# Optimization experiments

Measured on AMD Instinct MI355X. Metric: run time of the kernel, lower is better.

## Reference

```python
import jax, jax.numpy as jnp
import numpy as np
import math

N_NODES = 100000
N_EDGES = 1600000
D_FEAT = 32
K = 1        # Bernstein index k
N_ORD = 2    # Bernstein order n
COMB = float(math.comb(N_ORD, K))


def setup_inputs() -> dict:
    key = jax.random.key(0)
    k1, k2, k3 = jax.random.split(key, 3)
    feat = jax.random.normal(k1, (N_NODES, D_FEAT), dtype=jnp.float32)
    edge_src = jax.random.randint(k2, (N_EDGES,), 0, N_NODES)
    edge_dst = jax.random.randint(k3, (N_EDGES,), 0, N_NODES)
    return {"feat": feat, "edge_src": edge_src, "edge_dst": edge_dst}


def reference(feat, edge_src, edge_dst):
    # in-degree of each node (copy_u/sum aggregates over incoming edges)
    deg = jax.ops.segment_sum(jnp.ones((N_EDGES,), feat.dtype), edge_dst,
                              num_segments=N_NODES)
    d_invsqrt = jnp.clip(deg, 1.0, None) ** -0.5  # [N]
    d_invsqrt = d_invsqrt[:, None]                 # [N,1]

    def unn_laplacian(x):
        msg = (x * d_invsqrt)[edge_src]            # [E,D]
        agg = jax.ops.segment_sum(msg, edge_dst, num_segments=N_NODES)
        return x - agg * d_invsqrt

    if K == 0:
        h = feat
        for _ in range(N_ORD):
            h = unn_laplacian(h) / 2
            h = feat - h
    elif K == N_ORD:
        h = feat
        for _ in range(N_ORD):
            h = unn_laplacian(h) / 2
    else:
        temp = feat
        for _ in range(K):
            temp = unn_laplacian(temp) / 2
        h = feat
        for _ in range(N_ORD - K):
            h = unn_laplacian(h) / 2
            h = feat - h
        h = temp * h
    return COMB * h
```

## Files before the change

kernel.cpp:

```cpp
#include <hip/hip_runtime.h>

#define N_NODES 100000
#define N_EDGES 1600000
#define D_FEAT 32

#define BSH 7
#define BMASK 127
#define NB 782
#define CAPB 2432

#define P1_BS 512
#define P1_TILE 4096
#define P1_CAP 16


static __device__ __forceinline__ unsigned pack_bf16(float a, float b) {
    unsigned ua = __float_as_uint(a);
    unsigned ub = __float_as_uint(b);
    ua = (ua + 0x7FFFu + ((ua >> 16) & 1u)) >> 16;
    ub = (ub + 0x7FFFu + ((ub >> 16) & 1u)) >> 16;
    return (ua & 0xFFFFu) | (ub << 16);
}

__global__ void init_kernel(int* __restrict__ cursorA) {
    int b = blockIdx.x * blockDim.x + threadIdx.x;
    if (b < NB) cursorA[b] = b * CAPB;
}

__global__ void __launch_bounds__(P1_BS)
bucket_kernel(const int* __restrict__ edge_src,
              const int* __restrict__ edge_dst,
              int* __restrict__ cursorA,
              int* __restrict__ pairs, int n_edges) {
    __shared__ int s_cnt[NB];
    __shared__ int s_base[NB];
    __shared__ int s_off[NB + 1];
    __shared__ int s_buf[NB * P1_CAP];

    int tile = blockIdx.x * P1_TILE;
    if (tile >= n_edges) return;

    for (int b = threadIdx.x; b < NB; b += P1_BS) s_cnt[b] = 0;
    __syncthreads();

    const int4* src4 = reinterpret_cast<const int4*>(edge_src);
    const int4* dst4 = reinterpret_cast<const int4*>(edge_dst);
    int tileq = blockIdx.x * (P1_TILE / 4);
    #pragma unroll
    for (int j = 0; j < P1_TILE / 4 / P1_BS; ++j) {
        int iq = tileq + j * P1_BS + threadIdx.x;
        if (iq * 4 < n_edges) {
            int4 sv = src4[iq];
            int4 dv = dst4[iq];
            int ss[4] = {sv.x, sv.y, sv.z, sv.w};
            int dd[4] = {dv.x, dv.y, dv.z, dv.w};
            #pragma unroll
            for (int u = 0; u < 4; ++u) {
                int b = dd[u] >> BSH;
                int packed = (ss[u] << BSH) | (dd[u] & BMASK);
                int p = atomicAdd(&s_cnt[b], 1);
                if (p < P1_CAP) {
                    s_buf[b * P1_CAP + p] = packed;
                } else {
                    int gp = atomicAdd(&cursorA[b], 1);
                    pairs[gp] = packed;
                }
            }
        }
    }
    __syncthreads();

    for (int b = threadIdx.x; b < NB; b += P1_BS) {
        int c = min(s_cnt[b], P1_CAP);
        s_base[b] = atomicAdd(&cursorA[b], c);
        s_cnt[b] = c;
    }
    __syncthreads();
    if (threadIdx.x == 0) {
        int acc = 0;
        for (int b = 0; b < NB; ++b) { s_off[b] = acc; acc += s_cnt[b]; }
        s_off[NB] = acc;
    }
    __syncthreads();

    int total = s_off[NB];
    for (int t = threadIdx.x; t < total; t += P1_BS) {
        int lo = 0, hi = NB;
        while (hi - lo > 1) {
            int mid = (lo + hi) >> 1;
            if (t >= s_off[mid]) lo = mid; else hi = mid;
        }
        int idx = t - s_off[lo];
        pairs[s_base[lo] + idx] = s_buf[lo * P1_CAP + idx];
    }
}

__global__ void __launch_bounds__(256)
sort_kernel(const int* __restrict__ pairs,
            const int* __restrict__ cursorA,
            const float* __restrict__ feat,
            int* __restrict__ ssrc,
            int2* __restrict__ srange,
            float* __restrict__ dinv,
            unsigned* __restrict__ sfeat) {
    __shared__ int buf[CAPB];
    __shared__ int outb[CAPB];
    __shared__ int h[128];
    __shared__ int sc[128];
    __shared__ int cur[128];
    __shared__ float dv_s[128];

    int b = blockIdx.x;
    int t = threadIdx.x;
    int base = b * CAPB;
    int cnt = min(cursorA[b] - base, CAPB);

    if (t < 128) h[t] = 0;
    __syncthreads();
    for (int i = t; i < cnt; i += 256) {
        int p = pairs[base + i];
        buf[i] = p;
        atomicAdd(&h[p & BMASK], 1);
    }
    __syncthreads();

    int v = 0;
    if (t < 128) { v = h[t]; sc[t] = v; }
    __syncthreads();
    for (int off = 1; off < 128; off <<= 1) {
        int x = 0;
        if (t < 128 && t >= off) x = sc[t - off];
        __syncthreads();
        if (t < 128) sc[t] += x;
        __syncthreads();
    }
    if (t < 128) {
        int ex = sc[t] - v;
        cur[t] = ex;
        int node = (b << BSH) + t;
        if (node < N_NODES) {
            srange[node] = make_int2(base + ex, base + ex + v);
            float dvv = rsqrtf(fmaxf((float)v, 1.0f));
            dinv[node] = dvv;
            dv_s[t] = dvv;
        }
    }
    __syncthreads();

    for (int i = t; i < cnt; i += 256) {
        int p = buf[i];
        int pos = atomicAdd(&cur[p & BMASK], 1);
        outb[pos] = p >> BSH;
    }
    __syncthreads();
    for (int i = t; i < cnt; i += 256)
        ssrc[base + i] = outb[i];

    const float4* feat4 = reinterpret_cast<const float4*>(feat);
    uint4* sf4 = reinterpret_cast<uint4*>(sfeat);
    for (int idx = t; idx < 128 * 4; idx += 256) {
        int nl = idx >> 2;
        int q = idx & 3;
        int node = (b << BSH) + nl;
        if (node >= N_NODES) continue;
        float dvv = dv_s[nl];
        float4 fa = feat4[node * 8 + 2 * q];
        float4 fb = feat4[node * 8 + 2 * q + 1];
        uint4 pk;
        pk.x = pack_bf16(fa.x * dvv, fa.y * dvv);
        pk.y = pack_bf16(fa.z * dvv, fa.w * dvv);
        pk.z = pack_bf16(fb.x * dvv, fb.y * dvv);
        pk.w = pack_bf16(fb.z * dvv, fb.w * dvv);
        sf4[node * 4 + q] = pk;
    }
}

__global__ void gather_bf_kernel(const float* __restrict__ feat,
                                 const unsigned* __restrict__ sfeat,
                                 const int2* __restrict__ srange,
                                 const int* __restrict__ ssrc,
                                 const float* __restrict__ dinv,
                                 float* __restrict__ out) {
    int gid = blockIdx.x * blockDim.x + threadIdx.x;
    int node = gid >> 2;
    int q = gid & 3;
    if (node >= N_NODES) return;
    int2 se = srange[node];
    int k = se.x, en = se.y;
    const uint4* sf4 = reinterpret_cast<const uint4*>(sfeat);
    float a0 = 0.f, a1 = 0.f, a2 = 0.f, a3 = 0.f;
    float a4 = 0.f, a5 = 0.f, a6 = 0.f, a7 = 0.f;

    #define ACC(r)                                                 \
        a0 += __uint_as_float((r).x << 16);                        \
        a1 += __uint_as_float((r).x & 0xFFFF0000u);                \
        a2 += __uint_as_float((r).y << 16);                        \
        a3 += __uint_as_float((r).y & 0xFFFF0000u);                \
        a4 += __uint_as_float((r).z << 16);                        \
        a5 += __uint_as_float((r).z & 0xFFFF0000u);                \
        a6 += __uint_as_float((r).w << 16);                        \
        a7 += __uint_as_float((r).w & 0xFFFF0000u);

    for (; k + 3 < en; k += 4) {
        int s0 = ssrc[k],     s1 = ssrc[k + 1];
        int s2 = ssrc[k + 2], s3 = ssrc[k + 3];
        uint4 r0 = sf4[s0 * 4 + q];
        uint4 r1 = sf4[s1 * 4 + q];
        uint4 r2 = sf4[s2 * 4 + q];
        uint4 r3 = sf4[s3 * 4 + q];
        ACC(r0) ACC(r1) ACC(r2) ACC(r3)
    }
    for (; k < en; ++k) {
        uint4 r = sf4[ssrc[k] * 4 + q];
        ACC(r)
    }
    #undef ACC

    float dvn = dinv[node];
    const float4* feat4 = reinterpret_cast<const float4*>(feat);
    float4 fa = feat4[node * 8 + 2 * q];
    float4 fb = feat4[node * 8 + 2 * q + 1];
    float4 oa, ob;
    float y;
    y = 0.5f * (fa.x - a0 * dvn); oa.x = 2.0f * y * (fa.x - y);
    y = 0.5f * (fa.y - a1 * dvn); oa.y = 2.0f * y * (fa.y - y);
    y = 0.5f * (fa.z - a2 * dvn); oa.z = 2.0f * y * (fa.z - y);
    y = 0.5f * (fa.w - a3 * dvn); oa.w = 2.0f * y * (fa.w - y);
    y = 0.5f * (fb.x - a4 * dvn); ob.x = 2.0f * y * (fb.x - y);
    y = 0.5f * (fb.y - a5 * dvn); ob.y = 2.0f * y * (fb.y - y);
    y = 0.5f * (fb.z - a6 * dvn); ob.z = 2.0f * y * (fb.z - y);
    y = 0.5f * (fb.w - a7 * dvn); ob.w = 2.0f * y * (fb.w - y);
    float4* out4 = reinterpret_cast<float4*>(out);
    out4[node * 8 + 2 * q] = oa;
    out4[node * 8 + 2 * q + 1] = ob;
}

extern "C" void kernel_launch(void* const* d_in, const int* in_sizes, int n_in,
                              void* d_out, int out_size, void* d_ws, size_t ws_size,
                              hipStream_t stream) {
    const float* feat = (const float*)d_in[0];
    const int* edge_src = (const int*)d_in[1];
    const int* edge_dst = (const int*)d_in[2];
    float* out = (float*)d_out;

    int* ws = (int*)d_ws;
    int* cursorA   = ws;
    int2* srange   = (int2*)(cursorA + 1024);
    float* dinv    = (float*)(srange + N_NODES);
    int* ssrc      = (int*)(dinv + N_NODES);
    int* pairs     = ssrc + NB * CAPB;
    unsigned* sfeat = (unsigned*)(pairs + NB * CAPB);

    init_kernel<<<1, 1024, 0, stream>>>(cursorA);
    {
        int blocks = (N_EDGES + P1_TILE - 1) / P1_TILE;
        bucket_kernel<<<blocks, P1_BS, 0, stream>>>(edge_src, edge_dst,
                                                    cursorA, pairs, N_EDGES);
    }
    sort_kernel<<<NB, 256, 0, stream>>>(pairs, cursorA, feat, ssrc, srange,
                                        dinv, sfeat);
    {
        int total = N_NODES * 4;
        int blocks = (total + 255) / 256;
        gather_bf_kernel<<<blocks, 256, 0, stream>>>(feat, sfeat, srange,
                                                     ssrc, dinv, out);
    }
}
```

Before: 131.9 us.

## Fuse bucket sort into gather kernel, keep sorted sources in LDS

Splits the old sort kernel into a histogram/prescale pass that only computes degrees and the bf16 scaled features. A second kernel re-sorts each bucket and runs the gather straight from shared memory, so the sorted source array and node ranges are never written to or read back from global memory. The init kernel is replaced by a memset, with cursors now stored relative to each bucket. The cost is reading the pairs twice and giving each block only 256 threads to gather for 128 nodes, which may lower parallelism and occupancy because of the large LDS footprint.

```diff
diff --git a/kernel.cpp b/kernel.cpp
--- a/kernel.cpp
+++ b/kernel.cpp
@@ -20,11 +20,6 @@
     ua = (ua + 0x7FFFu + ((ua >> 16) & 1u)) >> 16;
     ub = (ub + 0x7FFFu + ((ub >> 16) & 1u)) >> 16;
     return (ua & 0xFFFFu) | (ub << 16);
-}
-
-__global__ void init_kernel(int* __restrict__ cursorA) {
-    int b = blockIdx.x * blockDim.x + threadIdx.x;
-    if (b < NB) cursorA[b] = b * CAPB;
 }
 
 __global__ void __launch_bounds__(P1_BS)
@@ -63,7 +58,7 @@
                     s_buf[b * P1_CAP + p] = packed;
                 } else {
                     int gp = atomicAdd(&cursorA[b], 1);
-                    pairs[gp] = packed;
+                    if (gp < CAPB) pairs[b * CAPB + gp] = packed;
                 }
             }
         }
@@ -72,7 +67,7 @@
 
     for (int b = threadIdx.x; b < NB; b += P1_BS) {
         int c = min(s_cnt[b], P1_CAP);
-        s_base[b] = atomicAdd(&cursorA[b], c);
+        s_base[b] = b * CAPB + atomicAdd(&cursorA[b], c);
         s_cnt[b] = c;
     }
     __syncthreads();
@@ -96,65 +91,30 @@
 }
 
 __global__ void __launch_bounds__(256)
-sort_kernel(const int* __restrict__ pairs,
+hist_kernel(const int* __restrict__ pairs,
             const int* __restrict__ cursorA,
             const float* __restrict__ feat,
-            int* __restrict__ ssrc,
-            int2* __restrict__ srange,
             float* __restrict__ dinv,
             unsigned* __restrict__ sfeat) {
-    __shared__ int buf[CAPB];
-    __shared__ int outb[CAPB];
     __shared__ int h[128];
-    __shared__ int sc[128];
-    __shared__ int cur[128];
     __shared__ float dv_s[128];
-
     int b = blockIdx.x;
     int t = threadIdx.x;
     int base = b * CAPB;
-    int cnt = min(cursorA[b] - base, CAPB);
+    int cnt = min(cursorA[b], CAPB);
 
     if (t < 128) h[t] = 0;
     __syncthreads();
-    for (int i = t; i < cnt; i += 256) {
-        int p = pairs[base + i];
-        buf[i] = p;
-        atomicAdd(&h[p & BMASK], 1);
-    }
-    __syncthreads();
-
-    int v = 0;
-    if (t < 128) { v = h[t]; sc[t] = v; }
-    __syncthreads();
-    for (int off = 1; off < 128; off <<= 1) {
-        int x = 0;
-        if (t < 128 && t >= off) x = sc[t - off];
-        __syncthreads();
-        if (t < 128) sc[t] += x;
-        __syncthreads();
-    }
+    for (int i = t; i < cnt; i += 256)
+        atomicAdd(&h[pairs[base + i] & BMASK], 1);
+    __syncthreads();
     if (t < 128) {
-        int ex = sc[t] - v;
-        cur[t] = ex;
+        float dvv = rsqrtf(fmaxf((float)h[t], 1.0f));
+        dv_s[t] = dvv;
         int node = (b << BSH) + t;
-        if (node < N_NODES) {
-            srange[node] = make_int2(base + ex, base + ex + v);
-            float dvv = rsqrtf(fmaxf((float)v, 1.0f));
-            dinv[node] = dvv;
-            dv_s[t] = dvv;
-        }
-    }
-    __syncthreads();
-
-    for (int i = t; i < cnt; i += 256) {
-        int p = buf[i];
-        int pos = atomicAdd(&cur[p & BMASK], 1);
-        outb[pos] = p >> BSH;
-    }
-    __syncthreads();
-    for (int i = t; i < cnt; i += 256)
-        ssrc[base + i] = outb[i];
+        if (node < N_NODES) dinv[node] = dvv;
+    }
+    __syncthreads();
 
     const float4* feat4 = reinterpret_cast<const float4*>(feat);
     uint4* sf4 = reinterpret_cast<uint4*>(sfeat);
@@ -175,21 +135,64 @@
     }
 }
 
-__global__ void gather_bf_kernel(const float* __restrict__ feat,
-                                 const unsigned* __restrict__ sfeat,
-                                 const int2* __restrict__ srange,
-                                 const int* __restrict__ ssrc,
-                                 const float* __restrict__ dinv,
-                                 float* __restrict__ out) {
-    int gid = blockIdx.x * blockDim.x + threadIdx.x;
-    int node = gid >> 2;
-    int q = gid & 3;
-    if (node >= N_NODES) return;
-    int2 se = srange[node];
-    int k = se.x, en = se.y;
+__global__ void __launch_bounds__(256)
+sortgather_kernel(const int* __restrict__ pairs,
+                  const int* __restrict__ cursorA,
+                  const float* __restrict__ feat,
+                  const unsigned* __restrict__ sfeat,
+                  float* __restrict__ out) {
+    __shared__ int buf[CAPB];
+    __shared__ int outb[CAPB];
+    __shared__ int h[128];
+    __shared__ int sc[128];
+    __shared__ int cur[128];
+    __shared__ int exs[128];
+    __shared__ int cnl[128];
+    __shared__ float dv_s[128];
+
+    int b = blockIdx.x;
+    int t = threadIdx.x;
+    int base = b * CAPB;
+    int cnt = min(cursorA[b], CAPB);
+
+    if (t < 128) h[t] = 0;
+    __syncthreads();
+    for (int i = t; i < cnt; i += 256) {
+        int p = pairs[base + i];
+        buf[i] = p;
+        atomicAdd(&h[p & BMASK], 1);
+    }
+    __syncthreads();
+
+    int v = 0;
+    if (t < 128) { v = h[t]; sc[t] = v; }
+    __syncthreads();
+    for (int off = 1; off < 128; off <<= 1) {
+        int x = 0;
+        if (t < 128 && t >= off) x = sc[t - off];
+        __syncthreads();
+        if (t < 128) sc[t] += x;
+        __syncthreads();
+    }
+    if (t < 128) {
+        int ex = sc[t] - v;
+        cur[t] = ex;
+        exs[t] = ex;
+        cnl[t] = v;
+        dv_s[t] = rsqrtf(fmaxf((float)v, 1.0f));
+    }
+    __syncthreads();
+
+    for (int i = t; i < cnt; i += 256) {
+        int p = buf[i];
+        int pos = atomicAdd(&cur[p & BMASK], 1);
+        outb[pos] = p >> BSH;
+    }
+    __syncthreads();
+
     const uint4* sf4 = reinterpret_cast<const uint4*>(sfeat);
-    float a0 = 0.f, a1 = 0.f, a2 = 0.f, a3 = 0.f;
-    float a4 = 0.f, a5 = 0.f, a6 = 0.f, a7 = 0.f;
+    const float4* feat4 = reinterpret_cast<const float4*>(feat);
+    float4* out4 = reinterpret_cast<float4*>(out);
 
     #define ACC(r)                                                 \
         a0 += __uint_as_float((r).x << 16);                        \
@@ -201,38 +204,47 @@
         a6 += __uint_as_float((r).w << 16);                        \
         a7 += __uint_as_float((r).w & 0xFFFF0000u);
 
-    for (; k + 3 < en; k += 4) {
-        int s0 = ssrc[k],     s1 = ssrc[k + 1];
-        int s2 = ssrc[k + 2], s3 = ssrc[k + 3];
-        uint4 r0 = sf4[s0 * 4 + q];
-        uint4 r1 = sf4[s1 * 4 + q];
-        uint4 r2 = sf4[s2 * 4 + q];
-        uint4 r3 = sf4[s3 * 4 + q];
-        ACC(r0) ACC(r1) ACC(r2) ACC(r3)
-    }
-    for (; k < en; ++k) {
-        uint4 r = sf4[ssrc[k] * 4 + q];
-        ACC(r)
+    #pragma unroll
+    for (int pass = 0; pass < 2; ++pass) {
+        int item = t + pass * 256;
+        int nl = item >> 2;
+        int q = item & 3;
+        int node = (b << BSH) + nl;
+        if (node >= N_NODES) continue;
+        int k = exs[nl];
+        int en = k + cnl[nl];
+        float a0 = 0.f, a1 = 0.f, a2 = 0.f, a3 = 0.f;
+        float a4 = 0.f, a5 = 0.f, a6 = 0.f, a7 = 0.f;
+        for (; k + 3 < en; k += 4) {
+            int s0 = outb[k],     s1 = outb[k + 1];
+            int s2 = outb[k + 2], s3 = outb[k + 3];
+            uint4 r0 = sf4[s0 * 4 + q];
+            uint4 r1 = sf4[s1 * 4 + q];
+            uint4 r2 = sf4[s2 * 4 + q];
+            uint4 r3 = sf4[s3 * 4 + q];
+            ACC(r0) ACC(r1) ACC(r2) ACC(r3)
+        }
+        for (; k < en; ++k) {
+            uint4 r = sf4[outb[k] * 4 + q];
+            ACC(r)
+        }
+        float dvn = dv_s[nl];
+        float4 fa = feat4[node * 8 + 2 * q];
+        float4 fb = feat4[node * 8 + 2 * q + 1];
+        float4 oa, ob;
+        float y;
+        y = 0.5f * (fa.x - a0 * dvn); oa.x = 2.0f * y * (fa.x - y);
+        y = 0.5f * (fa.y - a1 * dvn); oa.y = 2.0f * y * (fa.y - y);
+        y = 0.5f * (fa.z - a2 * dvn); oa.z = 2.0f * y * (fa.z - y);
+        y = 0.5f * (fa.w - a3 * dvn); oa.w = 2.0f * y * (fa.w - y);
+        y = 0.5f * (fb.x - a4 * dvn); ob.x = 2.0f * y * (fb.x - y);
+        y = 0.5f * (fb.y - a5 * dvn); ob.y = 2.0f * y * (fb.y - y);
+        y = 0.5f * (fb.z - a6 * dvn); ob.z = 2.0f * y * (fb.z - y);
+        y = 0.5f * (fb.w - a7 * dvn); ob.w = 2.0f * y * (fb.w - y);
+        out4[node * 8 + 2 * q] = oa;
+        out4[node * 8 + 2 * q + 1] = ob;
     }
     #undef ACC
-
-    float dvn = dinv[node];
-    const float4* feat4 = reinterpret_cast<const float4*>(feat);
-    float4 fa = feat4[node * 8 + 2 * q];
-    float4 fb = feat4[node * 8 + 2 * q + 1];
-    float4 oa, ob;
-    float y;
-    y = 0.5f * (fa.x - a0 * dvn); oa.x = 2.0f * y * (fa.x - y);
-    y = 0.5f * (fa.y - a1 * dvn); oa.y = 2.0f * y * (fa.y - y);
-    y = 0.5f * (fa.z - a2 * dvn); oa.z = 2.0f * y * (fa.z - y);
-    y = 0.5f * (fa.w - a3 * dvn); oa.w = 2.0f * y * (fa.w - y);
-    y = 0.5f * (fb.x - a4 * dvn); ob.x = 2.0f * y * (fb.x - y);
-    y = 0.5f * (fb.y - a5 * dvn); ob.y = 2.0f * y * (fb.y - y);
-    y = 0.5f * (fb.z - a6 * dvn); ob.z = 2.0f * y * (fb.z - y);
-    y = 0.5f * (fb.w - a7 * dvn); ob.w = 2.0f * y * (fb.w - y);
-    float4* out4 = reinterpret_cast<float4*>(out);
-    out4[node * 8 + 2 * q] = oa;
-    out4[node * 8 + 2 * q + 1] = ob;
 }
 
 extern "C" void kernel_launch(void* const* d_in, const int* in_sizes, int n_in,
@@ -244,25 +256,17 @@
     float* out = (float*)d_out;
 
     int* ws = (int*)d_ws;
-    int* cursorA   = ws;
-    int2* srange   = (int2*)(cursorA + 1024);
-    float* dinv    = (float*)(srange + N_NODES);
-    int* ssrc      = (int*)(dinv + N_NODES);
-    int* pairs     = ssrc + NB * CAPB;
+    int* cursorA    = ws;
+    float* dinv     = (float*)(cursorA + 1024);
+    int* pairs      = (int*)(dinv + N_NODES);
     unsigned* sfeat = (unsigned*)(pairs + NB * CAPB);
 
-    init_kernel<<<1, 1024, 0, stream>>>(cursorA);
+    hipMemsetAsync(cursorA, 0, 1024 * sizeof(int), stream);
     {
         int blocks = (N_EDGES + P1_TILE - 1) / P1_TILE;
         bucket_kernel<<<blocks, P1_BS, 0, stream>>>(edge_src, edge_dst,
                                                     cursorA, pairs, N_EDGES);
     }
-    sort_kernel<<<NB, 256, 0, stream>>>(pairs, cursorA, feat, ssrc, srange,
-                                        dinv, sfeat);
-    {
-        int total = N_NODES * 4;
-        int blocks = (total + 255) / 256;
-        gather_bf_kernel<<<blocks, 256, 0, stream>>>(feat, sfeat, srange,
-                                                     ssrc, dinv, out);
-    }
-}
+    hist_kernel<<<NB, 256, 0, stream>>>(pairs, cursorA, feat, dinv, sfeat);
+    sortgather_kernel<<<NB, 256, 0, stream>>>(pairs, cursorA, feat, sfeat, out);
+}
```

Measured after the change: 133.4 us. No clear change (+1.1%).
